# Optimization experiments

Measured on AMD Instinct MI355X. Metric: run time of the kernel, lower is better.

The kernel has to match this reference:

```python
import jax, jax.numpy as jnp
import numpy as np

N = 50000        # nodes
E = 400000       # edges (no self-loops; self-loops appended in forward)
IN_DIM = 128
H, C = 4, 64     # heads, channels per head
D = H * C        # 256
NEG_SLOPE = 0.2


def setup_inputs() -> dict:
    key = jax.random.key(0)
    ks = jax.random.split(key, 8)
    x = jax.random.normal(ks[0], (N, IN_DIM), jnp.float32)
    # build edges with no self-loops (src != dst), matching the module's mask
    src = jax.random.randint(ks[1], (E,), 0, N)
    off = jax.random.randint(ks[2], (E,), 1, N)
    dst = (src + off) % N
    edge_index = jnp.stack([src, dst]).astype(jnp.int32)
    inp = {"x": x, "edge_index": edge_index}
    dims_in = [IN_DIM, D, D, D, D]
    for l in range(5):
        k = jax.random.split(ks[3 + l], 4)
        inp[f"W{l}"] = jax.random.normal(k[0], (D, dims_in[l]), jnp.float32) * 0.05
        inp[f"att_src{l}"] = jax.random.normal(k[1], (1, H, C), jnp.float32) * 0.05
        inp[f"att_dst{l}"] = jax.random.normal(k[2], (1, H, C), jnp.float32) * 0.05
        inp[f"bias{l}"] = jnp.zeros((D,), jnp.float32)
    return inp


def _gat_layer(x, W, a_src, a_dst, b, src, dst, relu_out):
    # linear projection, reshape to [N, H, C]
    h = (x @ W.T).reshape(N, H, C)
    alpha_src = jnp.sum(h * a_src, axis=-1)   # [N, H]
    alpha_dst = jnp.sum(h * a_dst, axis=-1)   # [N, H]
    # per-edge logits: alpha_j (source) + alpha_i (dest)
    alpha = jax.nn.leaky_relu(alpha_src[src] + alpha_dst[dst], negative_slope=NEG_SLOPE)  # [E', H]
    # segment softmax over destination neighborhoods (max is detached, as in the original)
    m = jax.lax.stop_gradient(jax.ops.segment_max(alpha, dst, num_segments=N))  # [N, H]
    e = jnp.exp(alpha - m[dst])
    s = jax.ops.segment_sum(e, dst, num_segments=N) + 1e-16
    a = e / s[dst]                                                             # [E', H]
    # weighted scatter-add aggregation of gathered source features
    out = jax.ops.segment_sum(a[:, :, None] * h[src], dst, num_segments=N)     # [N, H, C]
    out = out.reshape(N, D) + b
    return jax.nn.relu(out) if relu_out else out


def reference(x, edge_index,
              W0, att_src0, att_dst0, bias0,
              W1, att_src1, att_dst1, bias1,
              W2, att_src2, att_dst2, bias2,
              W3, att_src3, att_dst3, bias3,
              W4, att_src4, att_dst4, bias4):
    # input edges contain no self-loops; append one self-loop per node (as in the trace)
    loops = jnp.arange(N, dtype=edge_index.dtype)
    src = jnp.concatenate([edge_index[0], loops])
    dst = jnp.concatenate([edge_index[1], loops])
    params = [(W0, att_src0, att_dst0, bias0), (W1, att_src1, att_dst1, bias1),
              (W2, att_src2, att_dst2, bias2), (W3, att_src3, att_dst3, bias3),
              (W4, att_src4, att_dst4, bias4)]
    h = x
    for l, (W, a_s, a_d, b) in enumerate(params):
        h = _gat_layer(h, W, a_s, a_d, b, src, dst, relu_out=(l < 4))
    return h
```

## Files before the change

kernel.cpp:

```cpp
#include <hip/hip_runtime.h>
#include <hip/hip_bf16.h>

#define H 4
#define D 256
#define NEG_SLOPE 0.2f

typedef __attribute__((ext_vector_type(8))) _Float16 f16x8;
typedef __attribute__((ext_vector_type(4))) _Float16 f16x4;
typedef __attribute__((ext_vector_type(4))) float f32x4;

template<int K>
__device__ __forceinline__ void cvt_wfrag_one(const float* __restrict__ W,
                                              _Float16* __restrict__ wfrag, int idx) {
    const int NKS = K / 32;
    if (idx >= 16 * NKS * 64) return;
    int l  = idx & 63;
    int ks = (idx >> 6) % NKS;
    int c16 = idx / (NKS * 64);
    int col = c16 * 16 + (l & 15);
    int k0  = ks * 32 + (l >> 4) * 8;
    const float* src = &W[(size_t)col * K + k0];
    float4 v0 = *(const float4*)src;
    float4 v1 = *(const float4*)(src + 4);
    f16x8 o = {(_Float16)v0.x, (_Float16)v0.y, (_Float16)v0.z, (_Float16)v0.w,
               (_Float16)v1.x, (_Float16)v1.y, (_Float16)v1.z, (_Float16)v1.w};
    *(f16x8*)&wfrag[(size_t)idx * 8] = o;
}

__global__ void k_cvt_wfrag0(const float* __restrict__ W, _Float16* __restrict__ wfrag) {
    cvt_wfrag_one<128>(W, wfrag, blockIdx.x * blockDim.x + threadIdx.x);
}

__global__ void k_cvt_wfrag_all(const float* __restrict__ w1, const float* __restrict__ w2,
                                const float* __restrict__ w3, const float* __restrict__ w4,
                                _Float16* __restrict__ wfrag) {
    const float* ws[4] = {w1, w2, w3, w4};
    int l = blockIdx.y;
    cvt_wfrag_one<256>(ws[l], wfrag + 128 * 256 + (size_t)l * 256 * 256,
                       blockIdx.x * blockDim.x + threadIdx.x);
}

template<int K, bool F32X>
__global__ __launch_bounds__(256) void k_gemm_mfma(
        const void* __restrict__ xin, const _Float16* __restrict__ wfrag,
        const float* __restrict__ att_src, const float* __restrict__ att_dst,
        _Float16* __restrict__ hmat, float* __restrict__ alpha_src,
        float* __restrict__ alpha_dst, int nrows, int nchunk) {
    const int NKS = K / 32;
    __shared__ _Float16 sw[4 * NKS * 64 * 8];
    int t = threadIdx.x;
    int w = t >> 6, l = t & 63;
    int r = l & 15, q = l >> 4;

    int bid = blockIdx.x;
    int nfull = (nchunk >> 3) << 3;
    int dmain = nfull * 4;
    int chunk, split;
    if (bid < dmain) {
        int j = bid >> 3;
        chunk = (bid & 7) + 8 * (j >> 2);
        split = j & 3;
    } else {
        int idx = bid - dmain;
        chunk = nfull + (idx >> 2);
        split = idx & 3;
    }
    int row0 = chunk * 64;

    {
        const uint4* wsrc = (const uint4*)(wfrag + (size_t)split * 4 * NKS * 64 * 8);
        uint4* wdst = (uint4*)sw;
        #pragma unroll
        for (int i = 0; i < NKS; ++i)
            wdst[i * 256 + t] = wsrc[i * 256 + t];
    }

    int gr_a = row0 + w * 16 + r;
    bool aok = (gr_a < nrows);
    f16x8 a[NKS];
    #pragma unroll
    for (int ks = 0; ks < NKS; ++ks) {
        if (aok) {
            if constexpr (F32X) {
                const float* xs = (const float*)xin + (size_t)gr_a * K + ks * 32 + q * 8;
                float4 v0 = *(const float4*)xs;
                float4 v1 = *(const float4*)(xs + 4);
                a[ks] = (f16x8){(_Float16)v0.x, (_Float16)v0.y, (_Float16)v0.z,
                                (_Float16)v0.w, (_Float16)v1.x, (_Float16)v1.y,
                                (_Float16)v1.z, (_Float16)v1.w};
            } else {
                a[ks] = *(const f16x8*)((const _Float16*)xin + (size_t)gr_a * K + ks * 32 + q * 8);
            }
        } else {
            a[ks] = (f16x8){0, 0, 0, 0, 0, 0, 0, 0};
        }
    }

    __syncthreads();

    f32x4 acc[4];
    #pragma unroll
    for (int cf = 0; cf < 4; ++cf) acc[cf] = (f32x4){0.f, 0.f, 0.f, 0.f};
    #pragma unroll
    for (int cf = 0; cf < 4; ++cf) {
        f16x8 b[NKS];
        #pragma unroll
        for (int ks = 0; ks < NKS; ++ks)
            b[ks] = *(f16x8*)&sw[(size_t)((cf * NKS + ks) * 64 + l) * 8];
        #pragma unroll
        for (int ks = 0; ks < NKS; ++ks)
            acc[cf] = __builtin_amdgcn_mfma_f32_16x16x32_f16(a[ks], b[ks], acc[cf], 0, 0, 0);
    }

    #pragma unroll
    for (int cf = 0; cf < 4; ++cf) {
        #pragma unroll
        for (int i = 0; i < 4; ++i) {
            int gr = row0 + w * 16 + q * 4 + i;
            if (gr < nrows)
                hmat[(size_t)gr * D + split * 64 + cf * 16 + r] = (_Float16)acc[cf][i];
        }
    }
    float asv[4], adv[4];
    #pragma unroll
    for (int cf = 0; cf < 4; ++cf) {
        asv[cf] = att_src[split * 64 + cf * 16 + r];
        adv[cf] = att_dst[split * 64 + cf * 16 + r];
    }
    #pragma unroll
    for (int i = 0; i < 4; ++i) {
        float ps = 0.f, pd = 0.f;
        #pragma unroll
        for (int cf = 0; cf < 4; ++cf) {
            ps += acc[cf][i] * asv[cf];
            pd += acc[cf][i] * adv[cf];
        }
        #pragma unroll
        for (int m = 1; m < 16; m <<= 1) {
            ps += __shfl_xor(ps, m);
            pd += __shfl_xor(pd, m);
        }
        int gr = row0 + w * 16 + q * 4 + i;
        if (r == 0 && gr < nrows) {
            alpha_src[gr * 4 + split] = ps;
            alpha_dst[gr * 4 + split] = pd;
        }
    }
}

__global__ void k_deg(const int* __restrict__ ei, int E, int E2, int* __restrict__ deg) {
    int e = blockIdx.x * blockDim.x + threadIdx.x;
    if (e >= E2) return;
    int de = (e < E) ? ei[E + e] : (e - E);
    atomicAdd(&deg[de], 1);
}

__global__ void k_scan_block(const int* __restrict__ deg, int* __restrict__ incl,
                             int* __restrict__ bsum, int n) {
    __shared__ int sd[256];
    int t = threadIdx.x;
    int i = blockIdx.x * 256 + t;
    int v = (i < n) ? deg[i] : 0;
    sd[t] = v;
    __syncthreads();
    for (int off = 1; off < 256; off <<= 1) {
        int add = (t >= off) ? sd[t - off] : 0;
        __syncthreads();
        sd[t] += add;
        __syncthreads();
    }
    if (i < n) incl[i] = sd[t];
    if (t == 255) bsum[blockIdx.x] = sd[255];
}

__global__ void k_scan_bsum(int* __restrict__ bsum, int nb) {
    __shared__ int sd[256];
    int t = threadIdx.x;
    int v = (t < nb) ? bsum[t] : 0;
    sd[t] = v;
    __syncthreads();
    for (int off = 1; off < 256; off <<= 1) {
        int add = (t >= off) ? sd[t - off] : 0;
        __syncthreads();
        sd[t] += add;
        __syncthreads();
    }
    if (t < nb) bsum[t] = sd[t] - v;
}

__global__ void k_rowptr(const int* __restrict__ incl, const int* __restrict__ deg,
                         const int* __restrict__ boff, int* __restrict__ row_ptr,
                         int* __restrict__ cursor, int n, int total) {
    int i = blockIdx.x * blockDim.x + threadIdx.x;
    if (i < n) {
        row_ptr[i] = incl[i] - deg[i] + boff[i >> 8];
        cursor[i] = 0;
    }
    if (i == 0) row_ptr[n] = total;
}

__global__ void k_scatter(const int* __restrict__ ei, int E, int E2,
                          const int* __restrict__ row_ptr, int* __restrict__ cursor,
                          int* __restrict__ csr_src) {
    int e = blockIdx.x * blockDim.x + threadIdx.x;
    if (e >= E2) return;
    int se, de;
    if (e < E) { se = ei[e]; de = ei[E + e]; }
    else       { se = e - E; de = se; }
    int pos = atomicAdd(&cursor[de], 1);
    csr_src[row_ptr[de] + pos] = se;
}

__global__ __launch_bounds__(256) void k_aggregate(const _Float16* __restrict__ hmat,
        const int* __restrict__ row_ptr, const int* __restrict__ csr_src,
        const float* __restrict__ alpha_src, const float* __restrict__ alpha_dst,
        const float* __restrict__ bias, float* __restrict__ outf,
        _Float16* __restrict__ outx, int relu, int nrows) {
    int wid  = (blockIdx.x * 256 + threadIdx.x) >> 6;
    int lane = threadIdx.x & 63;
    int node = wid * 2 + (lane >> 5);
    if (node >= nrows) return;
    int c    = lane & 31;
    int head = c >> 3;
    int st = row_ptr[node], en = row_ptr[node + 1];
    int deg = en - st;
    int nbatch = (deg + 7) >> 3;
    float a_d = alpha_dst[node * 4 + head];
    float acc[8] = {};
    float ssum = 0.f;
    int sn[8];
    #pragma unroll
    for (int j = 0; j < 8; ++j) {
        int li = st + (j < deg ? j : deg - 1);
        sn[j] = csr_src[li];
    }
    for (int b = 0; b < nbatch; ++b) {
        f16x8 hv[8];
        #pragma unroll
        for (int j = 0; j < 8; ++j)
            hv[j] = *(const f16x8*)&hmat[(size_t)sn[j] * D + c * 8];
        float as[8];
        #pragma unroll
        for (int j = 0; j < 8; ++j) as[j] = alpha_src[sn[j] * 4 + head];
        int sn2[8];
        if (b + 1 < nbatch) {
            #pragma unroll
            for (int j = 0; j < 8; ++j) {
                int e = (b + 1) * 8 + j;
                int li = st + (e < deg ? e : deg - 1);
                sn2[j] = csr_src[li];
            }
        }
        #pragma unroll
        for (int j = 0; j < 8; ++j) {
            float a = as[j] + a_d;
            a = a > 0.f ? a : NEG_SLOPE * a;
            float ex = (b * 8 + j < deg) ? __expf(a) : 0.f;
            ssum += ex;
            #pragma unroll
            for (int k = 0; k < 8; ++k) acc[k] += ex * (float)hv[j][k];
        }
        #pragma unroll
        for (int j = 0; j < 8; ++j) sn[j] = sn2[j];
    }
    float sinv = 1.f / (ssum + 1e-16f);
    float4 b0 = *(const float4*)&bias[c * 8];
    float4 b1 = *(const float4*)&bias[c * 8 + 4];
    float o[8];
    o[0] = acc[0] * sinv + b0.x; o[1] = acc[1] * sinv + b0.y;
    o[2] = acc[2] * sinv + b0.z; o[3] = acc[3] * sinv + b0.w;
    o[4] = acc[4] * sinv + b1.x; o[5] = acc[5] * sinv + b1.y;
    o[6] = acc[6] * sinv + b1.z; o[7] = acc[7] * sinv + b1.w;
    if (relu) {
        #pragma unroll
        for (int k = 0; k < 8; ++k) o[k] = fmaxf(o[k], 0.f);
    }
    if (outx) {
        f16x8 o8 = {(_Float16)o[0], (_Float16)o[1], (_Float16)o[2], (_Float16)o[3],
                    (_Float16)o[4], (_Float16)o[5], (_Float16)o[6], (_Float16)o[7]};
        *(f16x8*)&outx[(size_t)node * D + c * 8] = o8;
    } else {
        *(float4*)&outf[(size_t)node * D + c * 8] =
            make_float4(o[0], o[1], o[2], o[3]);
        *(float4*)&outf[(size_t)node * D + c * 8 + 4] =
            make_float4(o[4], o[5], o[6], o[7]);
    }
}

extern "C" void kernel_launch(void* const* d_in, const int* in_sizes, int n_in,
                              void* d_out, int out_size, void* d_ws, size_t ws_size,
                              hipStream_t stream) {
    const float* x = (const float*)d_in[0];
    const int* ei = (const int*)d_in[1];
    const int N  = in_sizes[0] / 128;
    const int E  = in_sizes[1] / 2;
    const int E2 = E + N;

    char* wsp = (char*)d_ws;
    size_t off = 0;
    auto alloc = [&](size_t bytes) -> void* {
        void* p = wsp + off;
        off += (bytes + 255) & ~(size_t)255;
        return p;
    };
    _Float16* bufH  = (_Float16*)alloc((size_t)N * D * 2);
    _Float16* xf16  = (_Float16*)alloc((size_t)N * D * 2);
    _Float16* wfrag = (_Float16*)alloc((size_t)(128 * 256 + 4 * 256 * 256) * 2);
    float* alpha_src = (float*)alloc((size_t)N * H * 4);
    float* alpha_dst = (float*)alloc((size_t)N * H * 4);
    int*   deg       = (int*)alloc((size_t)N * 4);
    int*   incl      = (int*)alloc((size_t)N * 4);
    int*   bsum      = (int*)alloc(256 * 4);
    int*   row_ptr   = (int*)alloc((size_t)(N + 1) * 4);
    int*   cursor    = (int*)alloc((size_t)N * 4);
    int*   csr_src   = (int*)alloc((size_t)E2 * 4);
    (void)ws_size;

    hipMemsetAsync(deg, 0, (size_t)N * 4, stream);

    k_cvt_wfrag0<<<(16 * 4 * 64 + 255) / 256, 256, 0, stream>>>(
        (const float*)d_in[2], wfrag);
    dim3 wg((16 * 8 * 64 + 255) / 256, 4);
    k_cvt_wfrag_all<<<wg, 256, 0, stream>>>(
        (const float*)d_in[6], (const float*)d_in[10],
        (const float*)d_in[14], (const float*)d_in[18], wfrag);

    int egrid = (E2 + 255) / 256;
    k_deg<<<egrid, 256, 0, stream>>>(ei, E, E2, deg);
    int nb = (N + 255) / 256;
    k_scan_block<<<nb, 256, 0, stream>>>(deg, incl, bsum, N);
    k_scan_bsum<<<1, 256, 0, stream>>>(bsum, nb);
    k_rowptr<<<nb, 256, 0, stream>>>(incl, deg, bsum, row_ptr, cursor, N, E2);
    k_scatter<<<egrid, 256, 0, stream>>>(ei, E, E2, row_ptr, cursor, csr_src);

    int nchunk = (N + 63) / 64;
    int ggrid = nchunk * 4;
    int agrid = (N + 7) / 8;
    for (int l = 0; l < 5; ++l) {
        const float* as_ = (const float*)d_in[3 + 4 * l];
        const float* ad_ = (const float*)d_in[4 + 4 * l];
        const float* bs_ = (const float*)d_in[5 + 4 * l];
        const _Float16* wl = (l == 0) ? wfrag
                           : wfrag + 128 * 256 + (size_t)(l - 1) * 256 * 256;

        if (l == 0)
            k_gemm_mfma<128, true><<<ggrid, 256, 0, stream>>>(x, wl, as_, ad_,
                                                        bufH, alpha_src, alpha_dst, N, nchunk);
        else
            k_gemm_mfma<256, false><<<ggrid, 256, 0, stream>>>(xf16, wl, as_, ad_,
                                                        bufH, alpha_src, alpha_dst, N, nchunk);

        int last = (l == 4);
        k_aggregate<<<agrid, 256, 0, stream>>>(bufH, row_ptr, csr_src,
                                               alpha_src, alpha_dst, bs_,
                                               last ? (float*)d_out : nullptr,
                                               last ? nullptr : xf16,
                                               last ? 0 : 1, N);
    }
}
```

Measured before the change: 374.5 us.

## Fuse aggregation of layer l with GEMM of layer l+1 via LDS tile

Adds a fused kernel in which each 256-thread block aggregates 64 destination nodes into a swizzled LDS tile, then immediately runs the next layer's MFMA projection and attention-logit reductions on it. This removes the fp16 intermediate write/read round trip through global memory and one launch per layer, at the cost of ping-pong h/alpha buffers. It also reduces the grid from nchunk*4 GEMM blocks to nchunk blocks with 32KB LDS each, so occupancy and parallelism drop. The gather phase now runs serially over 8 passes per block before any GEMM work starts.

After: 408.0 us. 1.09x slower.

```diff
diff --git a/kernel.cpp b/kernel.cpp
--- a/kernel.cpp
+++ b/kernel.cpp
@@ -148,6 +148,157 @@
     }
 }
 
+__global__ __launch_bounds__(256) void k_fused(
+        const _Float16* __restrict__ hin,
+        const int* __restrict__ row_ptr, const int* __restrict__ csr_src,
+        const float* __restrict__ asrc, const float* __restrict__ adst,
+        const float* __restrict__ bias,
+        const _Float16* __restrict__ wfrag,
+        const float* __restrict__ att_s, const float* __restrict__ att_d,
+        _Float16* __restrict__ hout,
+        float* __restrict__ asrc_o, float* __restrict__ adst_o,
+        int nrows) {
+    __shared__ _Float16 sx[64 * 256];
+    int t = threadIdx.x;
+    int w = t >> 6, lane = t & 63;
+    int row0 = blockIdx.x * 64;
+
+    {
+        int c    = lane & 31;
+        int half = lane >> 5;
+        int head = c >> 3;
+        for (int p = 0; p < 8; ++p) {
+            int nloc = p * 8 + w * 2 + half;
+            int node = row0 + nloc;
+            float o[8] = {0.f, 0.f, 0.f, 0.f, 0.f, 0.f, 0.f, 0.f};
+            if (node < nrows) {
+                int st = row_ptr[node], en = row_ptr[node + 1];
+                int deg = en - st;
+                int nbatch = (deg + 7) >> 3;
+                float a_d = adst[node * 4 + head];
+                float acc[8] = {};
+                float ssum = 0.f;
+                int sn[8];
+                #pragma unroll
+                for (int j = 0; j < 8; ++j) {
+                    int li = st + (j < deg ? j : deg - 1);
+                    sn[j] = csr_src[li];
+                }
+                for (int b = 0; b < nbatch; ++b) {
+                    f16x8 hv[8];
+                    #pragma unroll
+                    for (int j = 0; j < 8; ++j)
+                        hv[j] = *(const f16x8*)&hin[(size_t)sn[j] * D + c * 8];
+                    float as[8];
+                    #pragma unroll
+                    for (int j = 0; j < 8; ++j) as[j] = asrc[sn[j] * 4 + head];
+                    int sn2[8];
+                    if (b + 1 < nbatch) {
+                        #pragma unroll
+                        for (int j = 0; j < 8; ++j) {
+                            int e = (b + 1) * 8 + j;
+                            int li = st + (e < deg ? e : deg - 1);
+                            sn2[j] = csr_src[li];
+                        }
+                    }
+                    #pragma unroll
+                    for (int j = 0; j < 8; ++j) {
+                        float a = as[j] + a_d;
+                        a = a > 0.f ? a : NEG_SLOPE * a;
+                        float ex = (b * 8 + j < deg) ? __expf(a) : 0.f;
+                        ssum += ex;
+                        #pragma unroll
+                        for (int k = 0; k < 8; ++k) acc[k] += ex * (float)hv[j][k];
+                    }
+                    #pragma unroll
+                    for (int j = 0; j < 8; ++j) sn[j] = sn2[j];
+                }
+                float sinv = 1.f / (ssum + 1e-16f);
+                #pragma unroll
+                for (int k = 0; k < 8; ++k)
+                    o[k] = fmaxf(acc[k] * sinv + bias[c * 8 + k], 0.f);
+            }
+            f16x8 o8 = {(_Float16)o[0], (_Float16)o[1], (_Float16)o[2], (_Float16)o[3],
+                        (_Float16)o[4], (_Float16)o[5], (_Float16)o[6], (_Float16)o[7]};
+            int byte = nloc * 512 + ((c * 16) ^ ((nloc & 7) << 4));
+            *(f16x8*)((char*)sx + byte) = o8;
+        }
+    }
+    __syncthreads();
+
+    {
+        int r = lane & 15, q = lane >> 4;
+        f32x4 acc[4][4];
+        #pragma unroll
+        for (int rf = 0; rf < 4; ++rf)
+            #pragma unroll
+            for (int cf = 0; cf < 4; ++cf)
+                acc[rf][cf] = (f32x4){0.f, 0.f, 0.f, 0.f};
+
+        #pragma unroll
+        for (int rf = 0; rf < 4; ++rf) {
+            f16x8 a[8];
+            #pragma unroll
+            for (int ks = 0; ks < 8; ++ks) {
+                int n  = rf * 16 + r;
+                int cb = ks * 4 + q;
+                int byte = n * 512 + ((cb * 16) ^ ((n & 7) << 4));
+                a[ks] = *(f16x8*)((char*)sx + byte);
+            }
+            #pragma unroll
+            for (int cf = 0; cf < 4; ++cf) {
+                const _Float16* wp = wfrag + (size_t)((w * 4 + cf) * 8) * 64 * 8;
+                #pragma unroll
+                for (int ks = 0; ks < 8; ++ks) {
+                    f16x8 b = *(const f16x8*)&wp[(size_t)(ks * 64 + lane) * 8];
+                    acc[rf][cf] = __builtin_amdgcn_mfma_f32_16x16x32_f16(a[ks], b, acc[rf][cf], 0, 0, 0);
+                }
+            }
+        }
+
+        #pragma unroll
+        for (int rf = 0; rf < 4; ++rf) {
+            #pragma unroll
+            for (int cf = 0; cf < 4; ++cf) {
+                #pragma unroll
+                for (int i = 0; i < 4; ++i) {
+                    int gr = row0 + rf * 16 + q * 4 + i;
+                    if (gr < nrows)
+                        hout[(size_t)gr * D + w * 64 + cf * 16 + r] = (_Float16)acc[rf][cf][i];
+                }
+            }
+        }
+        float asv[4], adv[4];
+        #pragma unroll
+        for (int cf = 0; cf < 4; ++cf) {
+            asv[cf] = att_s[w * 64 + cf * 16 + r];
+            adv[cf] = att_d[w * 64 + cf * 16 + r];
+        }
+        #pragma unroll
+        for (int rf = 0; rf < 4; ++rf) {
+            #pragma unroll
+            for (int i = 0; i < 4; ++i) {
+                float ps = 0.f, pd = 0.f;
+                #pragma unroll
+                for (int cf = 0; cf < 4; ++cf) {
+                    ps += acc[rf][cf][i] * asv[cf];
+                    pd += acc[rf][cf][i] * adv[cf];
+                }
+                #pragma unroll
+                for (int m = 1; m < 16; m <<= 1) {
+                    ps += __shfl_xor(ps, m);
+                    pd += __shfl_xor(pd, m);
+                }
+                int gr = row0 + rf * 16 + q * 4 + i;
+                if (r == 0 && gr < nrows) {
+                    asrc_o[gr * 4 + w] = ps;
+                    adst_o[gr * 4 + w] = pd;
+                }
+            }
+        }
+    }
+}
+
 __global__ void k_deg(const int* __restrict__ ei, int E, int E2, int* __restrict__ deg) {
     int e = blockIdx.x * blockDim.x + threadIdx.x;
     if (e >= E2) return;
@@ -214,8 +365,7 @@
 __global__ __launch_bounds__(256) void k_aggregate(const _Float16* __restrict__ hmat,
         const int* __restrict__ row_ptr, const int* __restrict__ csr_src,
         const float* __restrict__ alpha_src, const float* __restrict__ alpha_dst,
-        const float* __restrict__ bias, float* __restrict__ outf,
-        _Float16* __restrict__ outx, int relu, int nrows) {
+        const float* __restrict__ bias, float* __restrict__ outf, int nrows) {
     int wid  = (blockIdx.x * 256 + threadIdx.x) >> 6;
     int lane = threadIdx.x & 63;
     int node = wid * 2 + (lane >> 5);
@@ -266,25 +416,12 @@
     float sinv = 1.f / (ssum + 1e-16f);
     float4 b0 = *(const float4*)&bias[c * 8];
     float4 b1 = *(const float4*)&bias[c * 8 + 4];
-    float o[8];
-    o[0] = acc[0] * sinv + b0.x; o[1] = acc[1] * sinv + b0.y;
-    o[2] = acc[2] * sinv + b0.z; o[3] = acc[3] * sinv + b0.w;
-    o[4] = acc[4] * sinv + b1.x; o[5] = acc[5] * sinv + b1.y;
-    o[6] = acc[6] * sinv + b1.z; o[7] = acc[7] * sinv + b1.w;
-    if (relu) {
-        #pragma unroll
-        for (int k = 0; k < 8; ++k) o[k] = fmaxf(o[k], 0.f);
-    }
-    if (outx) {
-        f16x8 o8 = {(_Float16)o[0], (_Float16)o[1], (_Float16)o[2], (_Float16)o[3],
-                    (_Float16)o[4], (_Float16)o[5], (_Float16)o[6], (_Float16)o[7]};
-        *(f16x8*)&outx[(size_t)node * D + c * 8] = o8;
-    } else {
-        *(float4*)&outf[(size_t)node * D + c * 8] =
-            make_float4(o[0], o[1], o[2], o[3]);
-        *(float4*)&outf[(size_t)node * D + c * 8 + 4] =
-            make_float4(o[4], o[5], o[6], o[7]);
-    }
+    *(float4*)&outf[(size_t)node * D + c * 8] =
+        make_float4(acc[0] * sinv + b0.x, acc[1] * sinv + b0.y,
+                    acc[2] * sinv + b0.z, acc[3] * sinv + b0.w);
+    *(float4*)&outf[(size_t)node * D + c * 8 + 4] =
+        make_float4(acc[4] * sinv + b1.x, acc[5] * sinv + b1.y,
+                    acc[6] * sinv + b1.z, acc[7] * sinv + b1.w);
 }
 
 extern "C" void kernel_launch(void* const* d_in, const int* in_sizes, int n_in,
@@ -304,16 +441,18 @@
         return p;
     };
     _Float16* bufH  = (_Float16*)alloc((size_t)N * D * 2);
-    _Float16* xf16  = (_Float16*)alloc((size_t)N * D * 2);
+    _Float16* bufH2 = (_Float16*)alloc((size_t)N * D * 2);
     _Float16* wfrag = (_Float16*)alloc((size_t)(128 * 256 + 4 * 256 * 256) * 2);
-    float* alpha_src = (float*)alloc((size_t)N * H * 4);
-    float* alpha_dst = (float*)alloc((size_t)N * H * 4);
-    int*   deg       = (int*)alloc((size_t)N * 4);
-    int*   incl      = (int*)alloc((size_t)N * 4);
-    int*   bsum      = (int*)alloc(256 * 4);
-    int*   row_ptr   = (int*)alloc((size_t)(N + 1) * 4);
-    int*   cursor    = (int*)alloc((size_t)N * 4);
-    int*   csr_src   = (int*)alloc((size_t)E2 * 4);
+    float* aspA = (float*)alloc((size_t)N * H * 4);
+    float* adpA = (float*)alloc((size_t)N * H * 4);
+    float* aspB = (float*)alloc((size_t)N * H * 4);
+    float* adpB = (float*)alloc((size_t)N * H * 4);
+    int*   deg      = (int*)alloc((size_t)N * 4);
+    int*   incl     = (int*)alloc((size_t)N * 4);
+    int*   bsum     = (int*)alloc(256 * 4);
+    int*   row_ptr  = (int*)alloc((size_t)(N + 1) * 4);
+    int*   cursor   = (int*)alloc((size_t)N * 4);
+    int*   csr_src  = (int*)alloc((size_t)E2 * 4);
     (void)ws_size;
 
     hipMemsetAsync(deg, 0, (size_t)N * 4, stream);
@@ -334,27 +473,26 @@
     k_scatter<<<egrid, 256, 0, stream>>>(ei, E, E2, row_ptr, cursor, csr_src);
 
     int nchunk = (N + 63) / 64;
-    int ggrid = nchunk * 4;
-    int agrid = (N + 7) / 8;
-    for (int l = 0; l < 5; ++l) {
-        const float* as_ = (const float*)d_in[3 + 4 * l];
-        const float* ad_ = (const float*)d_in[4 + 4 * l];
-        const float* bs_ = (const float*)d_in[5 + 4 * l];
-        const _Float16* wl = (l == 0) ? wfrag
-                           : wfrag + 128 * 256 + (size_t)(l - 1) * 256 * 256;
-
-        if (l == 0)
-            k_gemm_mfma<128, true><<<ggrid, 256, 0, stream>>>(x, wl, as_, ad_,
-                                                        bufH, alpha_src, alpha_dst, N, nchunk);
-        else
-            k_gemm_mfma<256, false><<<ggrid, 256, 0, stream>>>(xf16, wl, as_, ad_,
-                                                        bufH, alpha_src, alpha_dst, N, nchunk);
-
-        int last = (l == 4);
-        k_aggregate<<<agrid, 256, 0, stream>>>(bufH, row_ptr, csr_src,
-                                               alpha_src, alpha_dst, bs_,
-                                               last ? (float*)d_out : nullptr,
-                                               last ? nullptr : xf16,
-                                               last ? 0 : 1, N);
-    }
-}
+
+    k_gemm_mfma<128, true><<<nchunk * 4, 256, 0, stream>>>(
+        x, wfrag, (const float*)d_in[3], (const float*)d_in[4],
+        bufH, aspA, adpA, N, nchunk);
+
+    _Float16* hbuf[2] = {bufH, bufH2};
+    float* asp[2] = {aspA, aspB};
+    float* adp[2] = {adpA, adpB};
+    for (int l = 0; l < 4; ++l) {
+        int src = l & 1, dst = src ^ 1;
+        k_fused<<<nchunk, 256, 0, stream>>>(
+            hbuf[src], row_ptr, csr_src, asp[src], adp[src],
+            (const float*)d_in[5 + 4 * l],
+            wfrag + 128 * 256 + (size_t)l * 256 * 256,
+            (const float*)d_in[3 + 4 * (l + 1)],
+            (const float*)d_in[4 + 4 * (l + 1)],
+            hbuf[dst], asp[dst], adp[dst], N);
+    }
+
+    k_aggregate<<<(N + 7) / 8, 256, 0, stream>>>(
+        hbuf[0], row_ptr, csr_src, asp[0], adp[0],
+        (const float*)d_in[21], (float*)d_out, N);
+}
```

## Precompute edge softmax weights and split aggregation by column group

Applied to the files above, without the earlier changes.

Adds a per-node edge kernel that computes exp'd attention weights for all four heads and their inverse sums, stored head-major. Aggregation then uses grid blocks over 8 column groups of 32 channels. Within each, 4 lanes split edges and partial sums are reduced with shuffles. This spreads gather work over more blocks and drops the per-channel recomputation of exp. In exchange it adds a kernel launch per layer, an edge-weight array written and read back, and index reloads repeated across the 8 column-group blocks.

New measurement: 545.8 us. +45.8%, slower.

```diff
diff --git a/kernel.cpp b/kernel.cpp
--- a/kernel.cpp
+++ b/kernel.cpp
@@ -211,79 +211,89 @@
     csr_src[row_ptr[de] + pos] = se;
 }
 
-__global__ __launch_bounds__(256) void k_aggregate(const _Float16* __restrict__ hmat,
+__global__ void k_edge(const int* __restrict__ row_ptr, const int* __restrict__ csr_src,
+                       const float4* __restrict__ asp4, const float4* __restrict__ adp4,
+                       float* __restrict__ ew, float4* __restrict__ spinv,
+                       int E2, int n) {
+    int node = blockIdx.x * blockDim.x + threadIdx.x;
+    if (node >= n) return;
+    float4 ad = adp4[node];
+    int st = row_ptr[node], en = row_ptr[node + 1];
+    float4 s = make_float4(0.f, 0.f, 0.f, 0.f);
+    for (int i = st; i < en; ++i) {
+        float4 as = asp4[csr_src[i]];
+        float a; float4 w;
+        a = as.x + ad.x; a = a > 0.f ? a : NEG_SLOPE * a; w.x = __expf(a);
+        a = as.y + ad.y; a = a > 0.f ? a : NEG_SLOPE * a; w.y = __expf(a);
+        a = as.z + ad.z; a = a > 0.f ? a : NEG_SLOPE * a; w.z = __expf(a);
+        a = as.w + ad.w; a = a > 0.f ? a : NEG_SLOPE * a; w.w = __expf(a);
+        ew[i]          = w.x;
+        ew[E2 + i]     = w.y;
+        ew[2 * E2 + i] = w.z;
+        ew[3 * E2 + i] = w.w;
+        s.x += w.x; s.y += w.y; s.z += w.z; s.w += w.w;
+    }
+    spinv[node] = make_float4(1.f / (s.x + 1e-16f), 1.f / (s.y + 1e-16f),
+                              1.f / (s.z + 1e-16f), 1.f / (s.w + 1e-16f));
+}
+
+__global__ __launch_bounds__(256) void k_agg8(
+        const _Float16* __restrict__ hmat,
         const int* __restrict__ row_ptr, const int* __restrict__ csr_src,
-        const float* __restrict__ alpha_src, const float* __restrict__ alpha_dst,
+        const float* __restrict__ ew, const float* __restrict__ spinv,
         const float* __restrict__ bias, float* __restrict__ outf,
-        _Float16* __restrict__ outx, int relu, int nrows) {
-    int wid  = (blockIdx.x * 256 + threadIdx.x) >> 6;
-    int lane = threadIdx.x & 63;
-    int node = wid * 2 + (lane >> 5);
+        _Float16* __restrict__ outx, int E2, int relu, int nrows) {
+    int bid = blockIdx.x;
+    int cg = bid & 7;
+    int chunk = bid >> 3;
+    int t = threadIdx.x;
+    int w = t >> 6, lane = t & 63;
+    int node2 = lane >> 4;
+    int e4 = (lane >> 2) & 3;
+    int cq = lane & 3;
+    int node = chunk * 16 + w * 4 + node2;
     if (node >= nrows) return;
-    int c    = lane & 31;
-    int head = c >> 3;
+    int head = cg >> 1;
+    const float* ewp = ew + (size_t)head * E2;
     int st = row_ptr[node], en = row_ptr[node + 1];
     int deg = en - st;
-    int nbatch = (deg + 7) >> 3;
-    float a_d = alpha_dst[node * 4 + head];
     float acc[8] = {};
-    float ssum = 0.f;
-    int sn[8];
-    #pragma unroll
-    for (int j = 0; j < 8; ++j) {
-        int li = st + (j < deg ? j : deg - 1);
-        sn[j] = csr_src[li];
-    }
-    for (int b = 0; b < nbatch; ++b) {
-        f16x8 hv[8];
-        #pragma unroll
-        for (int j = 0; j < 8; ++j)
-            hv[j] = *(const f16x8*)&hmat[(size_t)sn[j] * D + c * 8];
-        float as[8];
-        #pragma unroll
-        for (int j = 0; j < 8; ++j) as[j] = alpha_src[sn[j] * 4 + head];
-        int sn2[8];
-        if (b + 1 < nbatch) {
+    for (int e = e4; e < deg; e += 4) {
+        int li = st + e;
+        int sn = csr_src[li];
+        float wgt = ewp[li];
+        f16x8 hv = *(const f16x8*)&hmat[(size_t)sn * D + cg * 32 + cq * 8];
+        #pragma unroll
+        for (int k = 0; k < 8; ++k) acc[k] += wgt * (float)hv[k];
+    }
+    #pragma unroll
+    for (int k = 0; k < 8; ++k) {
+        acc[k] += __shfl_xor(acc[k], 4);
+        acc[k] += __shfl_xor(acc[k], 8);
+    }
+    if (e4 == 0) {
+        float sinv = spinv[node * 4 + head];
+        float4 b0 = *(const float4*)&bias[cg * 32 + cq * 8];
+        float4 b1 = *(const float4*)&bias[cg * 32 + cq * 8 + 4];
+        float o[8];
+        o[0] = acc[0] * sinv + b0.x; o[1] = acc[1] * sinv + b0.y;
+        o[2] = acc[2] * sinv + b0.z; o[3] = acc[3] * sinv + b0.w;
+        o[4] = acc[4] * sinv + b1.x; o[5] = acc[5] * sinv + b1.y;
+        o[6] = acc[6] * sinv + b1.z; o[7] = acc[7] * sinv + b1.w;
+        if (relu) {
             #pragma unroll
-            for (int j = 0; j < 8; ++j) {
-                int e = (b + 1) * 8 + j;
-                int li = st + (e < deg ? e : deg - 1);
-                sn2[j] = csr_src[li];
-            }
-        }
-        #pragma unroll
-        for (int j = 0; j < 8; ++j) {
-            float a = as[j] + a_d;
-            a = a > 0.f ? a : NEG_SLOPE * a;
-            float ex = (b * 8 + j < deg) ? __expf(a) : 0.f;
-            ssum += ex;
-            #pragma unroll
-            for (int k = 0; k < 8; ++k) acc[k] += ex * (float)hv[j][k];
-        }
-        #pragma unroll
-        for (int j = 0; j < 8; ++j) sn[j] = sn2[j];
-    }
-    float sinv = 1.f / (ssum + 1e-16f);
-    float4 b0 = *(const float4*)&bias[c * 8];
-    float4 b1 = *(const float4*)&bias[c * 8 + 4];
-    float o[8];
-    o[0] = acc[0] * sinv + b0.x; o[1] = acc[1] * sinv + b0.y;
-    o[2] = acc[2] * sinv + b0.z; o[3] = acc[3] * sinv + b0.w;
-    o[4] = acc[4] * sinv + b1.x; o[5] = acc[5] * sinv + b1.y;
-    o[6] = acc[6] * sinv + b1.z; o[7] = acc[7] * sinv + b1.w;
-    if (relu) {
-        #pragma unroll
-        for (int k = 0; k < 8; ++k) o[k] = fmaxf(o[k], 0.f);
-    }
-    if (outx) {
-        f16x8 o8 = {(_Float16)o[0], (_Float16)o[1], (_Float16)o[2], (_Float16)o[3],
-                    (_Float16)o[4], (_Float16)o[5], (_Float16)o[6], (_Float16)o[7]};
-        *(f16x8*)&outx[(size_t)node * D + c * 8] = o8;
-    } else {
-        *(float4*)&outf[(size_t)node * D + c * 8] =
-            make_float4(o[0], o[1], o[2], o[3]);
-        *(float4*)&outf[(size_t)node * D + c * 8 + 4] =
-            make_float4(o[4], o[5], o[6], o[7]);
+            for (int k = 0; k < 8; ++k) o[k] = fmaxf(o[k], 0.f);
+        }
+        if (outx) {
+            f16x8 o8 = {(_Float16)o[0], (_Float16)o[1], (_Float16)o[2], (_Float16)o[3],
+                        (_Float16)o[4], (_Float16)o[5], (_Float16)o[6], (_Float16)o[7]};
+            *(f16x8*)&outx[(size_t)node * D + cg * 32 + cq * 8] = o8;
+        } else {
+            *(float4*)&outf[(size_t)node * D + cg * 32 + cq * 8] =
+                make_float4(o[0], o[1], o[2], o[3]);
+            *(float4*)&outf[(size_t)node * D + cg * 32 + cq * 8 + 4] =
+                make_float4(o[4], o[5], o[6], o[7]);
+        }
     }
 }
 
@@ -308,12 +318,14 @@
     _Float16* wfrag = (_Float16*)alloc((size_t)(128 * 256 + 4 * 256 * 256) * 2);
     float* alpha_src = (float*)alloc((size_t)N * H * 4);
     float* alpha_dst = (float*)alloc((size_t)N * H * 4);
-    int*   deg       = (int*)alloc((size_t)N * 4);
-    int*   incl      = (int*)alloc((size_t)N * 4);
-    int*   bsum      = (int*)alloc(256 * 4);
-    int*   row_ptr   = (int*)alloc((size_t)(N + 1) * 4);
-    int*   cursor    = (int*)alloc((size_t)N * 4);
-    int*   csr_src   = (int*)alloc((size_t)E2 * 4);
+    float* ew    = (float*)alloc((size_t)4 * E2 * 4);
+    float* spinv = (float*)alloc((size_t)N * 4 * 4);
+    int*   deg      = (int*)alloc((size_t)N * 4);
+    int*   incl     = (int*)alloc((size_t)N * 4);
+    int*   bsum     = (int*)alloc(256 * 4);
+    int*   row_ptr  = (int*)alloc((size_t)(N + 1) * 4);
+    int*   cursor   = (int*)alloc((size_t)N * 4);
+    int*   csr_src  = (int*)alloc((size_t)E2 * 4);
     (void)ws_size;
 
     hipMemsetAsync(deg, 0, (size_t)N * 4, stream);
@@ -334,8 +346,8 @@
     k_scatter<<<egrid, 256, 0, stream>>>(ei, E, E2, row_ptr, cursor, csr_src);
 
     int nchunk = (N + 63) / 64;
-    int ggrid = nchunk * 4;
-    int agrid = (N + 7) / 8;
+    int ngrid = (N + 255) / 256;
+    int agrid = ((N + 15) / 16) * 8;
     for (int l = 0; l < 5; ++l) {
         const float* as_ = (const float*)d_in[3 + 4 * l];
         const float* ad_ = (const float*)d_in[4 + 4 * l];
@@ -344,17 +356,21 @@
                            : wfrag + 128 * 256 + (size_t)(l - 1) * 256 * 256;
 
         if (l == 0)
-            k_gemm_mfma<128, true><<<ggrid, 256, 0, stream>>>(x, wl, as_, ad_,
-                                                        bufH, alpha_src, alpha_dst, N, nchunk);
+            k_gemm_mfma<128, true><<<nchunk * 4, 256, 0, stream>>>(
+                x, wl, as_, ad_, bufH, alpha_src, alpha_dst, N, nchunk);
         else
-            k_gemm_mfma<256, false><<<ggrid, 256, 0, stream>>>(xf16, wl, as_, ad_,
-                                                        bufH, alpha_src, alpha_dst, N, nchunk);
+            k_gemm_mfma<256, false><<<nchunk * 4, 256, 0, stream>>>(
+                xf16, wl, as_, ad_, bufH, alpha_src, alpha_dst, N, nchunk);
+
+        k_edge<<<ngrid, 256, 0, stream>>>(row_ptr, csr_src,
+                                          (const float4*)alpha_src,
+                                          (const float4*)alpha_dst,
+                                          ew, (float4*)spinv, E2, N);
 
         int last = (l == 4);
-        k_aggregate<<<agrid, 256, 0, stream>>>(bufH, row_ptr, csr_src,
-                                               alpha_src, alpha_dst, bs_,
-                                               last ? (float*)d_out : nullptr,
-                                               last ? nullptr : xf16,
-                                               last ? 0 : 1, N);
-    }
-}
+        k_agg8<<<agrid, 256, 0, stream>>>(bufH, row_ptr, csr_src, ew, spinv, bs_,
+                                          last ? (float*)d_out : nullptr,
+                                          last ? nullptr : xf16,
+                                          E2, last ? 0 : 1, N);
+    }
+}
```
